# Kernel tuning notes

Hardware: AMD Instinct MI355X
Metric: run time of the kernel (lower is better)

The kernel has to match this reference:

```python
import jax, jax.numpy as jnp
import numpy as np

USER_NUM = 100000
ITEM_NUM = 50000
D = 64
E = 3200000
B = 16384


def setup_inputs() -> dict:
    key = jax.random.key(0)
    ks = jax.random.split(key, 12)
    user = jax.random.randint(ks[0], (B,), 0, USER_NUM)
    item_i = jax.random.randint(ks[1], (B,), 0, ITEM_NUM)
    item_j = jax.random.randint(ks[2], (B,), 0, ITEM_NUM)
    edge_u = jax.random.randint(ks[3], (E,), 0, USER_NUM)
    edge_i = jax.random.randint(ks[4], (E,), 0, ITEM_NUM)
    edge_val = jax.random.uniform(ks[5], (E,), dtype=jnp.float32)
    # nn.init.normal_(std=0.01)
    user_emb = 0.01 * jax.random.normal(ks[6], (USER_NUM, D), dtype=jnp.float32)
    item_emb = 0.01 * jax.random.normal(ks[7], (ITEM_NUM, D), dtype=jnp.float32)
    old_U_emb = 0.01 * jax.random.normal(ks[8], (USER_NUM, D), dtype=jnp.float32)
    old_I_emb = 0.01 * jax.random.normal(ks[9], (ITEM_NUM, D), dtype=jnp.float32)
    n_U = jax.random.uniform(ks[10], (USER_NUM,), dtype=jnp.float32)
    n_U = n_U / jnp.linalg.norm(n_U)  # pre_self normalizes by L2 norm
    n_I = jax.random.uniform(ks[11], (ITEM_NUM,), dtype=jnp.float32)
    n_I = n_I / jnp.linalg.norm(n_I)
    return {"user": user, "item_i": item_i, "item_j": item_j,
            "edge_u": edge_u, "edge_i": edge_i, "edge_val": edge_val,
            "user_emb": user_emb, "item_emb": item_emb,
            "old_U_emb": old_U_emb, "old_I_emb": old_I_emb,
            "n_U": n_U, "n_I": n_I}


def _spmm(seg_ids, gather_ids, vals, x, num_segments):
    # one hop of sparse adjacency @ dense embeddings: gather -> scale -> scatter-add
    msg = vals[:, None] * x[gather_ids]          # [E, D]
    return jax.ops.segment_sum(msg, seg_ids, num_segments=num_segments)


def reference(user, item_i, item_j, edge_u, edge_i, edge_val,
              user_emb, item_emb, old_U_emb, old_I_emb, n_U, n_I):
    # 3-hop LightGCN-style propagation over bipartite graph
    g1u = _spmm(edge_u, edge_i, edge_val, item_emb, USER_NUM)
    g1i = _spmm(edge_i, edge_u, edge_val, user_emb, ITEM_NUM)
    g2u = _spmm(edge_u, edge_i, edge_val, g1i, USER_NUM)
    g2i = _spmm(edge_i, edge_u, edge_val, g1u, ITEM_NUM)
    g3u = _spmm(edge_u, edge_i, edge_val, g2i, USER_NUM)
    g3i = _spmm(edge_i, edge_u, edge_val, g2u, ITEM_NUM)
    gcn_u = user_emb + 0.5 * g1u + (1.0 / 3.0) * g2u + 0.25 * g3u
    gcn_i = item_emb + 0.5 * g1i + (1.0 / 3.0) * g2i + 0.25 * g3i

    # BPR loss
    u = gcn_u[user]
    ii = gcn_i[item_i]
    ij = gcn_i[item_j]
    pred_i = jnp.sum(u * ii, axis=-1)
    pred_j = jnp.sum(u * ij, axis=-1)
    bpr = -jnp.mean(jax.nn.log_sigmoid(pred_i - pred_j))
    reg = 1e-4 * jnp.mean(jnp.sum(u ** 2 + ii ** 2 + ij ** 2, axis=-1))
    loss_bpr = bpr + reg

    # self-distillation loss (loss_self)
    Ud = jnp.linalg.norm(old_U_emb - gcn_u, axis=1)  # [USER_NUM]
    Id = jnp.linalg.norm(old_I_emb - gcn_i, axis=1)  # [ITEM_NUM]
    loss_self = jnp.dot(Ud, n_U) / USER_NUM + jnp.dot(Id, n_I) / ITEM_NUM

    return jnp.stack([loss_bpr, 100.0 * loss_self,
                      jnp.float32(1.0), jnp.float32(1.0)])
```

## Files before the change

kernel.cpp:

```cpp
#include <hip/hip_runtime.h>

#define USER_NUM 100000
#define ITEM_NUM 50000
#define DD 64
#define NEDGE 3200000
#define NB 16384
#define NSLOT 256

#define ATILE 4096
#define NTILE ((NEDGE + ATILE - 1) / ATILE)
#define USH 9
#define ISH 8
#define UBK ((USER_NUM + (1 << USH) - 1) >> USH)
#define IBK ((ITEM_NUM + (1 << ISH) - 1) >> ISH)
#define NBK (UBK + IBK)
#define CPAD 16
#define HIST_GRID 784

#define FP8_SCALE 64.0f

typedef float v2f __attribute__((ext_vector_type(2)));

__device__ __forceinline__ float waveReduceSum(float x) {
#pragma unroll
    for (int off = 32; off > 0; off >>= 1)
        x += __shfl_down(x, off, 64);
    return x;
}

__device__ __forceinline__ unsigned roundbf(unsigned y) {
    return (y + 0x7fffu + ((y >> 16) & 1u)) >> 16;
}

__device__ __forceinline__ void dec8(const uint2 b, float* f) {
    v2f f0 = __builtin_amdgcn_cvt_pk_f32_fp8(b.x, false);
    v2f f1 = __builtin_amdgcn_cvt_pk_f32_fp8(b.x, true);
    v2f f2 = __builtin_amdgcn_cvt_pk_f32_fp8(b.y, false);
    v2f f3 = __builtin_amdgcn_cvt_pk_f32_fp8(b.y, true);
    f[0] = f0.x; f[1] = f0.y; f[2] = f1.x; f[3] = f1.y;
    f[4] = f2.x; f[5] = f2.y; f[6] = f3.x; f[7] = f3.y;
}
__device__ __forceinline__ void fma8p(const uint2 b, const float v, v2f* a) {
    v2f f0 = __builtin_amdgcn_cvt_pk_f32_fp8(b.x, false);
    v2f f1 = __builtin_amdgcn_cvt_pk_f32_fp8(b.x, true);
    v2f f2 = __builtin_amdgcn_cvt_pk_f32_fp8(b.y, false);
    v2f f3 = __builtin_amdgcn_cvt_pk_f32_fp8(b.y, true);
    const v2f vv = {v, v};
    a[0] += vv * f0;
    a[1] += vv * f1;
    a[2] += vv * f2;
    a[3] += vv * f3;
}
__device__ __forceinline__ uint2 pack_fp8x8(const float* a) {
    int lo = 0, hi = 0;
    lo = __builtin_amdgcn_cvt_pk_fp8_f32(a[0], a[1], lo, false);
    lo = __builtin_amdgcn_cvt_pk_fp8_f32(a[2], a[3], lo, true);
    hi = __builtin_amdgcn_cvt_pk_fp8_f32(a[4], a[5], hi, false);
    hi = __builtin_amdgcn_cvt_pk_fp8_f32(a[6], a[7], hi, true);
    return make_uint2((unsigned)lo, (unsigned)hi);
}

__global__ void __launch_bounds__(256) cvt8_kernel(
    const float4* __restrict__ src, uint2* __restrict__ dst, int n8) {
    int t = blockIdx.x * blockDim.x + threadIdx.x;
    if (t < n8) {
        float4 a = src[2 * t], b = src[2 * t + 1];
        float f[8] = {a.x * FP8_SCALE, a.y * FP8_SCALE, a.z * FP8_SCALE, a.w * FP8_SCALE,
                      b.x * FP8_SCALE, b.y * FP8_SCALE, b.z * FP8_SCALE, b.w * FP8_SCALE};
        dst[t] = pack_fp8x8(f);
    }
}


__global__ void __launch_bounds__(256) coarse_hist(
    const int4* __restrict__ eu4, const int4* __restrict__ ei4,
    int* __restrict__ coarseCnt) {
    __shared__ int lc[NBK];
    const int t = threadIdx.x;
    for (int j = t; j < NBK; j += 256) lc[j] = 0;
    __syncthreads();
    for (int k = blockIdx.x * 256 + t; k < NEDGE / 4; k += HIST_GRID * 256) {
        int4 u = eu4[k];
        int4 i = ei4[k];
        atomicAdd(&lc[u.x >> USH], 1); atomicAdd(&lc[u.y >> USH], 1);
        atomicAdd(&lc[u.z >> USH], 1); atomicAdd(&lc[u.w >> USH], 1);
        atomicAdd(&lc[UBK + (i.x >> ISH)], 1); atomicAdd(&lc[UBK + (i.y >> ISH)], 1);
        atomicAdd(&lc[UBK + (i.z >> ISH)], 1); atomicAdd(&lc[UBK + (i.w >> ISH)], 1);
    }
    __syncthreads();
    for (int j = t; j < NBK; j += 256)
        if (lc[j]) atomicAdd(&coarseCnt[j * CPAD], lc[j]);
}

__global__ void __launch_bounds__(512) coarse_scan(
    const int* __restrict__ cnt, int* __restrict__ base, int* __restrict__ cur) {
    __shared__ int a[512];
    const int t = threadIdx.x;
    int v = (t < UBK) ? cnt[t * CPAD] : 0;
    a[t] = v;
    __syncthreads();
    for (int off = 1; off < 512; off <<= 1) {
        int x = (t >= off) ? a[t - off] : 0;
        __syncthreads();
        a[t] += x;
        __syncthreads();
    }
    if (t < UBK) { base[t] = a[t] - v; cur[t * CPAD] = a[t] - v; }
    __syncthreads();
    v = (t < IBK) ? cnt[(UBK + t) * CPAD] : 0;
    a[t] = v;
    __syncthreads();
    for (int off = 1; off < 512; off <<= 1) {
        int x = (t >= off) ? a[t - off] : 0;
        __syncthreads();
        a[t] += x;
        __syncthreads();
    }
    if (t < IBK) { base[UBK + t] = a[t] - v; cur[(UBK + t) * CPAD] = a[t] - v; }
}

__global__ void __launch_bounds__(256, 4) binA(
    const int* __restrict__ eu, const int* __restrict__ ei,
    const float* __restrict__ ev,
    int* __restrict__ ccur,
    int2* __restrict__ stU, int2* __restrict__ stI) {
    __shared__ int2 pay[ATILE];
    __shared__ unsigned char sbid[ATILE];
    __shared__ int hist[256];
    __shared__ int pscan[256];
    __shared__ int cursor[256];
    __shared__ int delta[256];

    const int t = threadIdx.x;
    const int dirI = blockIdx.y;
    const int tb = blockIdx.x * ATILE;
    const int n = min(ATILE, NEDGE - tb);
    const int* key = dirI ? ei : eu;
    const int SH = dirI ? ISH : USH;

    hist[t] = 0;
    __syncthreads();
    for (int k = t; k < n; k += 256)
        atomicAdd(&hist[key[tb + k] >> SH], 1);
    __syncthreads();
    pscan[t] = hist[t];
    __syncthreads();
    for (int off = 1; off < 256; off <<= 1) {
        int x = (t >= off) ? pscan[t - off] : 0;
        __syncthreads();
        pscan[t] += x;
        __syncthreads();
    }
    {
        const int c = hist[t];
        const int lst = pscan[t] - c;
        cursor[t] = lst;
        int gp = 0;
        if (c > 0) {
            int* gc = dirI ? (ccur + UBK * CPAD) : ccur;
            gp = atomicAdd(&gc[t * CPAD], c);
        }
        delta[t] = gp - lst;
    }
    __syncthreads();
    if (dirI == 0) {
        for (int k = t; k < n; k += 256) {
            const int e = tb + k;
            const int u = eu[e], i = ei[e];
            const int b = u >> USH;
            const int p = atomicAdd(&cursor[b], 1);
            pay[p] = make_int2(((u & ((1 << USH) - 1)) << 16) | i,
                               __float_as_int(ev[e]));
            sbid[p] = (unsigned char)b;
        }
    } else {
        for (int k = t; k < n; k += 256) {
            const int e = tb + k;
            const int u = eu[e], i = ei[e];
            const int b = i >> ISH;
            const int p = atomicAdd(&cursor[b], 1);
            pay[p] = make_int2(((i & ((1 << ISH) - 1)) << 17) | u,
                               __float_as_int(ev[e]));
            sbid[p] = (unsigned char)b;
        }
    }
    __syncthreads();
    int2* st = dirI ? stI : stU;
    for (int p = t; p < n; p += 256)
        st[delta[sbid[p]] + p] = pay[p];
}

__global__ void __launch_bounds__(256) binB(
    const int2* __restrict__ stU, const int2* __restrict__ stI,
    const int* __restrict__ base, const int* __restrict__ cnt,
    int* __restrict__ rpU, int* __restrict__ rpI,
    unsigned* __restrict__ ivU, unsigned* __restrict__ ivI) {
    __shared__ int h[512];
    const int t = threadIdx.x;
    const int b = blockIdx.x;
    if (b < UBK) {
        const int s = base[b], n = cnt[b * CPAD];
        const int dbase = b << USH;
        h[t] = 0; h[t + 256] = 0;
        __syncthreads();
        for (int p = s + t; p < s + n; p += 256)
            atomicAdd(&h[(unsigned)stU[p].x >> 16], 1);
        __syncthreads();
        int o0 = h[t], o1 = h[t + 256];
        for (int off = 1; off < 512; off <<= 1) {
            int x0 = (t >= off) ? h[t - off] : 0;
            int x1 = (t + 256 >= off) ? h[t + 256 - off] : 0;
            __syncthreads();
            h[t] += x0; h[t + 256] += x1;
            __syncthreads();
        }
        int e0 = s + h[t] - o0, e1 = s + h[t + 256] - o1;
        __syncthreads();
        h[t] = e0; h[t + 256] = e1;
        if (dbase + t < USER_NUM) rpU[dbase + t] = e0;
        if (dbase + 256 + t < USER_NUM) rpU[dbase + 256 + t] = e1;
        if (t == 0 && dbase + 512 >= USER_NUM) rpU[USER_NUM] = s + n;
        __syncthreads();
        for (int p = s + t; p < s + n; p += 256) {
            int2 en = stU[p];
            unsigned x = (unsigned)en.x;
            int pos = atomicAdd(&h[x >> 16], 1);
            unsigned bf = roundbf((unsigned)en.y);
            ivU[pos] = (bf << 16) | (x & 0xFFFFu);
        }
    } else {
        const int ib = b - UBK;
        const int s = base[b], n = cnt[b * CPAD];
        const int dbase = ib << ISH;
        h[t] = 0;
        __syncthreads();
        for (int p = s + t; p < s + n; p += 256)
            atomicAdd(&h[(unsigned)stI[p].x >> 17], 1);
        __syncthreads();
        int o0 = h[t];
        for (int off = 1; off < 256; off <<= 1) {
            int x0 = (t >= off) ? h[t - off] : 0;
            __syncthreads();
            h[t] += x0;
            __syncthreads();
        }
        int e0 = s + h[t] - o0;
        __syncthreads();
        h[t] = e0;
        if (dbase + t < ITEM_NUM) rpI[dbase + t] = e0;
        if (t == 0 && dbase + 256 >= ITEM_NUM) rpI[ITEM_NUM] = s + n;
        __syncthreads();
        for (int p = s + t; p < s + n; p += 256) {
            int2 en = stI[p];
            unsigned x = (unsigned)en.x;
            int pos = atomicAdd(&h[x >> 17], 1);
            unsigned v15 = roundbf((unsigned)en.y) & 0x7FFFu;
            ivI[pos] = (v15 << 17) | (x & 0x1FFFFu);
        }
    }
}

#define UW (USER_NUM / 8)
#define IW (ITEM_NUM / 8)

template<bool ISU>
__device__ __forceinline__ int xof(unsigned q) {
    return ISU ? (int)(q & 0xFFFFu) : (int)(q & 0x1FFFFu);
}
template<bool ISU>
__device__ __forceinline__ float vof(unsigned q) {
    return ISU ? __uint_as_float(q & 0xFFFF0000u)
               : __uint_as_float((q >> 17) << 16);
}

template<bool ISU, int N>
__device__ __forceinline__ void edge_block(
    const unsigned* __restrict__ iv, int t,
    const uint2* __restrict__ srcr, v2f* a0, v2f* a1) {
    unsigned q[N];
    uint2 b[N];
#pragma unroll
    for (int j = 0; j < N; j++) q[j] = iv[t + j];
#pragma unroll
    for (int j = 0; j < N; j++) b[j] = srcr[xof<ISU>(q[j]) * 8];
#pragma unroll
    for (int j = 0; j < N; j++) fma8p(b[j], vof<ISU>(q[j]), (j & 1) ? a1 : a0);
}

template<bool ISU>
__device__ __forceinline__ void row_accum_own(
    const int* __restrict__ rp, const unsigned* __restrict__ iv,
    const uint2* __restrict__ src, int row, int r, float* acc) {
    const int s = rp[row], e2 = rp[row + 1];
    const uint2* __restrict__ srcr = src + r;
    v2f a0[4] = {{0.f, 0.f}, {0.f, 0.f}, {0.f, 0.f}, {0.f, 0.f}};
    v2f a1[4] = {{0.f, 0.f}, {0.f, 0.f}, {0.f, 0.f}, {0.f, 0.f}};
    int t = s;
    for (; t + 15 < e2; t += 16) edge_block<ISU, 16>(iv, t, srcr, a0, a1);
    if (t + 7 < e2) { edge_block<ISU, 8>(iv, t, srcr, a0, a1); t += 8; }
    if (t + 3 < e2) { edge_block<ISU, 4>(iv, t, srcr, a0, a1); t += 4; }
    if (t + 1 < e2) { edge_block<ISU, 2>(iv, t, srcr, a0, a1); t += 2; }
    if (t < e2)     edge_block<ISU, 1>(iv, t, srcr, a0, a1);
#pragma unroll
    for (int k = 0; k < 4; k++) {
        const v2f sv = a0[k] + a1[k];
        acc[2 * k]     = sv.x;
        acc[2 * k + 1] = sv.y;
    }
}

__global__ void __launch_bounds__(256) gather_hop_f8(
    const int* __restrict__ rpU, const unsigned* __restrict__ ivU,
    const uint2* __restrict__ srcForU, uint2* __restrict__ outU,
    const int* __restrict__ rpI, const unsigned* __restrict__ ivI,
    const uint2* __restrict__ srcForI, uint2* __restrict__ outI) {
    const int lane = threadIdx.x & 63;
    const int sub = lane >> 3;
    const int r = lane & 7;
    const int wave = blockIdx.x * 4 + (threadIdx.x >> 6);
    float acc[8];
    if (wave < UW) {
        const int row = wave * 8 + sub;
        row_accum_own<true>(rpU, ivU, srcForU, row, r, acc);
        outU[row * 8 + r] = pack_fp8x8(acc);
    } else if (wave < UW + IW) {
        const int row = (wave - UW) * 8 + sub;
        row_accum_own<false>(rpI, ivI, srcForI, row, r, acc);
        outI[row * 8 + r] = pack_fp8x8(acc);
    }
}

__global__ void __launch_bounds__(256) gather_hop3(
    const int* __restrict__ rpU, const unsigned* __restrict__ ivU,
    const uint2* __restrict__ srcForU,
    const int* __restrict__ rpI, const unsigned* __restrict__ ivI,
    const uint2* __restrict__ srcForI,
    const float4* __restrict__ embU, const uint2* __restrict__ g1u,
    const uint2* __restrict__ g2u, float4* __restrict__ gcnU,
    const float4* __restrict__ embI, const uint2* __restrict__ g1i,
    const uint2* __restrict__ g2i, float4* __restrict__ gcnI,
    const float4* __restrict__ oldU4, const float4* __restrict__ oldI4,
    const float* __restrict__ nU, const float* __restrict__ nI,
    float* __restrict__ accs) {
    const int lane = threadIdx.x & 63;
    const int sub = lane >> 3;
    const int r = lane & 7;
    const int wave = blockIdx.x * 4 + (threadIdx.x >> 6);
    float acc[8];
    const float4* emb; const uint2* g1; const uint2* g2; float4* gcn; int row;
    const float4* old4; const float* nrm; bool isU;
    if (wave < UW) {
        row = wave * 8 + sub;
        row_accum_own<true>(rpU, ivU, srcForU, row, r, acc);
        emb = embU; g1 = g1u; g2 = g2u; gcn = gcnU;
        old4 = oldU4; nrm = nU; isU = true;
    } else if (wave < UW + IW) {
        row = (wave - UW) * 8 + sub;
        row_accum_own<false>(rpI, ivI, srcForI, row, r, acc);
        emb = embI; g1 = g1i; g2 = g2i; gcn = gcnI;
        old4 = oldI4; nrm = nI; isU = false;
    } else return;
    {
        const float C1 = 0.5f / FP8_SCALE;
        const float C2 = (1.0f / 3.0f) / FP8_SCALE;
        const float C3 = 0.25f / FP8_SCALE;
        float f1[8], f2[8];
        dec8(g1[row * 8 + r], f1);
        dec8(g2[row * 8 + r], f2);
        const float4 e0 = emb[row * 16 + 2 * r];
        const float4 e1 = emb[row * 16 + 2 * r + 1];
        float4 o0, o1;
        o0.x = e0.x + C1 * f1[0] + C2 * f2[0] + C3 * acc[0];
        o0.y = e0.y + C1 * f1[1] + C2 * f2[1] + C3 * acc[1];
        o0.z = e0.z + C1 * f1[2] + C2 * f2[2] + C3 * acc[2];
        o0.w = e0.w + C1 * f1[3] + C2 * f2[3] + C3 * acc[3];
        o1.x = e1.x + C1 * f1[4] + C2 * f2[4] + C3 * acc[4];
        o1.y = e1.y + C1 * f1[5] + C2 * f2[5] + C3 * acc[5];
        o1.z = e1.z + C1 * f1[6] + C2 * f2[6] + C3 * acc[6];
        o1.w = e1.w + C1 * f1[7] + C2 * f2[7] + C3 * acc[7];
        gcn[row * 16 + 2 * r] = o0;
        gcn[row * 16 + 2 * r + 1] = o1;
        const float4 d0 = old4[row * 16 + 2 * r];
        const float4 d1 = old4[row * 16 + 2 * r + 1];
        const float ex = d0.x - o0.x, ey = d0.y - o0.y;
        const float ez = d0.z - o0.z, ew = d0.w - o0.w;
        const float fx = d1.x - o1.x, fy = d1.y - o1.y;
        const float fz = d1.z - o1.z, fw = d1.w - o1.w;
        float ss = ex * ex + ey * ey + ez * ez + ew * ew
                 + fx * fx + fy * fy + fz * fz + fw * fw;
        ss += __shfl_xor(ss, 1, 64);
        ss += __shfl_xor(ss, 2, 64);
        ss += __shfl_xor(ss, 4, 64);
        float val = (r == 0) ? sqrtf(ss) * nrm[row] : 0.0f;
        val = waveReduceSum(val);
        if (lane == 0) {
            const int slot = wave & (NSLOT - 1);
            unsafeAtomicAdd(&accs[(isU ? 2 : 3) * NSLOT + slot], val);
        }
    }
}

__global__ void __launch_bounds__(256) bpr_loss(
    const int* __restrict__ user, const int* __restrict__ itemI,
    const int* __restrict__ itemJ,
    const float4* __restrict__ gcnU4, const float4* __restrict__ gcnI4,
    float* __restrict__ accs) {
    const int lane = threadIdx.x & 63;
    const int sub = lane >> 4;
    const int r = lane & 15;
    const int W = blockIdx.x * 4 + (threadIdx.x >> 6);
    const int NW = gridDim.x * 4;
    float accB = 0.0f, accR = 0.0f;
    for (int g = W; g < NB / 4; g += NW) {
        const int samp = g * 4 + sub;
        const int uu = user[samp], vi = itemI[samp], vj = itemJ[samp];
        const float4 u  = gcnU4[uu * 16 + r];
        const float4 xi = gcnI4[vi * 16 + r];
        const float4 xj = gcnI4[vj * 16 + r];
        float pi = u.x * xi.x + u.y * xi.y + u.z * xi.z + u.w * xi.w;
        float pj = u.x * xj.x + u.y * xj.y + u.z * xj.z + u.w * xj.w;
        float rg = u.x * u.x + u.y * u.y + u.z * u.z + u.w * u.w
                 + xi.x * xi.x + xi.y * xi.y + xi.z * xi.z + xi.w * xi.w
                 + xj.x * xj.x + xj.y * xj.y + xj.z * xj.z + xj.w * xj.w;
#pragma unroll
        for (int off = 1; off <= 8; off <<= 1) {
            pi += __shfl_xor(pi, off, 64);
            pj += __shfl_xor(pj, off, 64);
            rg += __shfl_xor(rg, off, 64);
        }
        if (r == 0) {
            const float x = pi - pj;
            accB += fmaxf(-x, 0.0f) + log1pf(expf(-fabsf(x)));
            accR += rg;
        }
    }
    accB = waveReduceSum(accB);
    accR = waveReduceSum(accR);
    if (lane == 0) {
        const int slot = W & (NSLOT - 1);
        unsafeAtomicAdd(&accs[0 * NSLOT + slot], accB);
        unsafeAtomicAdd(&accs[1 * NSLOT + slot], accR);
    }
}

__global__ void __launch_bounds__(64) finalize(const float* __restrict__ accs,
                                               float* __restrict__ out) {
    const int lane = threadIdx.x;
    float s[4];
#pragma unroll
    for (int k = 0; k < 4; k++) {
        float v = 0.0f;
        for (int j = lane; j < NSLOT; j += 64) v += accs[k * NSLOT + j];
        s[k] = waveReduceSum(v);
    }
    if (lane == 0) {
        const float loss_bpr = s[0] / NB + 1e-4f * (s[1] / NB);
        const float loss_self = s[2] / USER_NUM + s[3] / ITEM_NUM;
        out[0] = loss_bpr;
        out[1] = 100.0f * loss_self;
        out[2] = 1.0f;
        out[3] = 1.0f;
    }
}

extern "C" void kernel_launch(void* const* d_in, const int* in_sizes, int n_in,
                              void* d_out, int out_size, void* d_ws, size_t ws_size,
                              hipStream_t stream) {
    const int*   user     = (const int*)d_in[0];
    const int*   item_i   = (const int*)d_in[1];
    const int*   item_j   = (const int*)d_in[2];
    const int*   edge_u   = (const int*)d_in[3];
    const int*   edge_i   = (const int*)d_in[4];
    const float* edge_val = (const float*)d_in[5];
    const float* user_emb = (const float*)d_in[6];
    const float* item_emb = (const float*)d_in[7];
    const float* old_U    = (const float*)d_in[8];
    const float* old_I    = (const float*)d_in[9];
    const float* n_U      = (const float*)d_in[10];
    const float* n_I      = (const float*)d_in[11];
    float* out = (float*)d_out;

    char* base = (char*)d_ws;
    size_t off = 0;
    auto carve = [&](size_t bytes) {
        char* p = base + off;
        off += (bytes + 255) & ~(size_t)255;
        return p;
    };
    int*      coarseCnt = (int*)carve(NBK * CPAD * 4);
    float*    accs      = (float*)carve(4 * NSLOT * 4);
    size_t zero_bytes = off;
    int*      cbase = (int*)carve(NBK * 4);
    int*      ccur  = (int*)carve(NBK * CPAD * 4);
    int*      rpU   = (int*)carve((USER_NUM + 1) * 4);
    int*      rpI   = (int*)carve((ITEM_NUM + 1) * 4);
    unsigned* ivU   = (unsigned*)carve((size_t)NEDGE * 4);
    unsigned* ivI   = (unsigned*)carve((size_t)NEDGE * 4);
    uint2*    ebU8  = (uint2*)carve((size_t)USER_NUM * DD);
    uint2*    ebI8  = (uint2*)carve((size_t)ITEM_NUM * DD);
    uint2*    g1u8  = (uint2*)carve((size_t)USER_NUM * DD);
    uint2*    g1i8  = (uint2*)carve((size_t)ITEM_NUM * DD);
    uint2*    g2u8  = (uint2*)carve((size_t)USER_NUM * DD);
    uint2*    g2i8  = (uint2*)carve((size_t)ITEM_NUM * DD);
    int2*     stU   = (int2*)carve((size_t)NEDGE * 8);
    int2*     stI   = (int2*)carve((size_t)NEDGE * 8);
    float* gcnU = (float*)stU;
    float* gcnI = (float*)stI;

    hipMemsetAsync(d_ws, 0, zero_bytes, stream);

    const dim3 blk(256);

    cvt8_kernel<<<(USER_NUM * 8 + 255) / 256, blk, 0, stream>>>(
        (const float4*)user_emb, ebU8, USER_NUM * 8);
    cvt8_kernel<<<(ITEM_NUM * 8 + 255) / 256, blk, 0, stream>>>(
        (const float4*)item_emb, ebI8, ITEM_NUM * 8);

    coarse_hist<<<HIST_GRID, blk, 0, stream>>>((const int4*)edge_u,
                                               (const int4*)edge_i, coarseCnt);
    coarse_scan<<<1, 512, 0, stream>>>(coarseCnt, cbase, ccur);
    binA<<<dim3(NTILE, 2), blk, 0, stream>>>(edge_u, edge_i, edge_val,
                                             ccur, stU, stI);
    binB<<<NBK, blk, 0, stream>>>(stU, stI, cbase, coarseCnt, rpU, rpI, ivU, ivI);

    const int hop_waves = UW + IW;
    const int hop_grid = (hop_waves + 3) / 4;

    gather_hop_f8<<<hop_grid, blk, 0, stream>>>(rpU, ivU, ebI8, g1u8,
                                                rpI, ivI, ebU8, g1i8);
    gather_hop_f8<<<hop_grid, blk, 0, stream>>>(rpU, ivU, g1i8, g2u8,
                                                rpI, ivI, g1u8, g2i8);
    gather_hop3<<<hop_grid, blk, 0, stream>>>(
        rpU, ivU, g2i8, rpI, ivI, g2u8,
        (const float4*)user_emb, g1u8, g2u8, (float4*)gcnU,
        (const float4*)item_emb, g1i8, g2i8, (float4*)gcnI,
        (const float4*)old_U, (const float4*)old_I, n_U, n_I, accs);

    bpr_loss<<<128, blk, 0, stream>>>(user, item_i, item_j,
                                      (const float4*)gcnU, (const float4*)gcnI, accs);
    finalize<<<1, 64, 0, stream>>>(accs, out);
}
```

Measured before the change: 536.3 us.

## Sort rows by degree so each wave processes rows of similar length

```diff
diff --git a/kernel.cpp b/kernel.cpp
--- a/kernel.cpp
+++ b/kernel.cpp
@@ -16,6 +16,9 @@
 #define NBK (UBK + IBK)
 #define CPAD 16
 #define HIST_GRID 784
+#define PROWS 2048
+#define PBLK_U ((USER_NUM + PROWS - 1) / PROWS)
+#define PBLK_I ((ITEM_NUM + PROWS - 1) / PROWS)
 
 #define FP8_SCALE 64.0f
 
@@ -256,6 +259,96 @@
             int pos = atomicAdd(&h[x >> 17], 1);
             unsigned v15 = roundbf((unsigned)en.y) & 0x7FFFu;
             ivI[pos] = (v15 << 17) | (x & 0x1FFFFu);
+        }
+    }
+}
+
+
+__global__ void __launch_bounds__(256) perm_hist(
+    const int* __restrict__ rpU, const int* __restrict__ rpI,
+    int* __restrict__ bins) {
+    __shared__ int lb[512];
+    const int t = threadIdx.x;
+    for (int j = t; j < 512; j += 256) lb[j] = 0;
+    __syncthreads();
+    const int total = USER_NUM + ITEM_NUM;
+    for (int r = blockIdx.x * 256 + t; r < total; r += gridDim.x * 256) {
+        if (r < USER_NUM) {
+            const int d = rpU[r + 1] - rpU[r];
+            atomicAdd(&lb[255 - min(d, 255)], 1);
+        } else {
+            const int rr = r - USER_NUM;
+            const int d = rpI[rr + 1] - rpI[rr];
+            atomicAdd(&lb[256 + 255 - min(d, 255)], 1);
+        }
+    }
+    __syncthreads();
+    for (int j = t; j < 512; j += 256)
+        if (lb[j]) atomicAdd(&bins[j], lb[j]);
+}
+
+__global__ void __launch_bounds__(256) perm_scan(
+    const int* __restrict__ bins, int* __restrict__ gcur) {
+    __shared__ int a[256];
+    const int t = threadIdx.x;
+    int v = bins[t];
+    a[t] = v;
+    __syncthreads();
+    for (int off = 1; off < 256; off <<= 1) {
+        int x = (t >= off) ? a[t - off] : 0;
+        __syncthreads();
+        a[t] += x;
+        __syncthreads();
+    }
+    gcur[t * CPAD] = a[t] - v;
+    __syncthreads();
+    v = bins[256 + t];
+    a[t] = v;
+    __syncthreads();
+    for (int off = 1; off < 256; off <<= 1) {
+        int x = (t >= off) ? a[t - off] : 0;
+        __syncthreads();
+        a[t] += x;
+        __syncthreads();
+    }
+    gcur[(256 + t) * CPAD] = a[t] - v;
+}
+
+__global__ void __launch_bounds__(256) perm_scatter(
+    const int* __restrict__ rpU, const int* __restrict__ rpI,
+    int* __restrict__ gcur,
+    int* __restrict__ permU, int* __restrict__ permI) {
+    __shared__ int lh[256], lcur[256], ldelta[256];
+    const int t = threadIdx.x;
+    const int b = blockIdx.x;
+    const bool isU = b < PBLK_U;
+    const int r0 = (isU ? b : (b - PBLK_U)) * PROWS;
+    const int NR = isU ? USER_NUM : ITEM_NUM;
+    const int* __restrict__ rp = isU ? rpU : rpI;
+    int* __restrict__ perm = isU ? permU : permI;
+    int* __restrict__ cur = gcur + (isU ? 0 : 256 * CPAD);
+    lh[t] = 0; lcur[t] = 0;
+    __syncthreads();
+    for (int k = t; k < PROWS; k += 256) {
+        const int r = r0 + k;
+        if (r < NR) {
+            const int d = rp[r + 1] - rp[r];
+            atomicAdd(&lh[255 - min(d, 255)], 1);
+        }
+    }
+    __syncthreads();
+    {
+        const int c = lh[t];
+        ldelta[t] = c ? atomicAdd(&cur[t * CPAD], c) : 0;
+    }
+    __syncthreads();
+    for (int k = t; k < PROWS; k += 256) {
+        const int r = r0 + k;
+        if (r < NR) {
+            const int d = rp[r + 1] - rp[r];
+            const int bin = 255 - min(d, 255);
+            const int rank = atomicAdd(&lcur[bin], 1);
+            perm[ldelta[bin] + rank] = r;
         }
     }
 }
@@ -313,18 +406,19 @@
     const int* __restrict__ rpU, const unsigned* __restrict__ ivU,
     const uint2* __restrict__ srcForU, uint2* __restrict__ outU,
     const int* __restrict__ rpI, const unsigned* __restrict__ ivI,
-    const uint2* __restrict__ srcForI, uint2* __restrict__ outI) {
+    const uint2* __restrict__ srcForI, uint2* __restrict__ outI,
+    const int* __restrict__ permU, const int* __restrict__ permI) {
     const int lane = threadIdx.x & 63;
     const int sub = lane >> 3;
     const int r = lane & 7;
     const int wave = blockIdx.x * 4 + (threadIdx.x >> 6);
     float acc[8];
     if (wave < UW) {
-        const int row = wave * 8 + sub;
+        const int row = permU[wave * 8 + sub];
         row_accum_own<true>(rpU, ivU, srcForU, row, r, acc);
         outU[row * 8 + r] = pack_fp8x8(acc);
     } else if (wave < UW + IW) {
-        const int row = (wave - UW) * 8 + sub;
+        const int row = permI[(wave - UW) * 8 + sub];
         row_accum_own<false>(rpI, ivI, srcForI, row, r, acc);
         outI[row * 8 + r] = pack_fp8x8(acc);
     }
@@ -341,7 +435,8 @@
     const uint2* __restrict__ g2i, float4* __restrict__ gcnI,
     const float4* __restrict__ oldU4, const float4* __restrict__ oldI4,
     const float* __restrict__ nU, const float* __restrict__ nI,
-    float* __restrict__ accs) {
+    float* __restrict__ accs,
+    const int* __restrict__ permU, const int* __restrict__ permI) {
     const int lane = threadIdx.x & 63;
     const int sub = lane >> 3;
     const int r = lane & 7;
@@ -350,12 +445,12 @@
     const float4* emb; const uint2* g1; const uint2* g2; float4* gcn; int row;
     const float4* old4; const float* nrm; bool isU;
     if (wave < UW) {
-        row = wave * 8 + sub;
+        row = permU[wave * 8 + sub];
         row_accum_own<true>(rpU, ivU, srcForU, row, r, acc);
         emb = embU; g1 = g1u; g2 = g2u; gcn = gcnU;
         old4 = oldU4; nrm = nU; isU = true;
     } else if (wave < UW + IW) {
-        row = (wave - UW) * 8 + sub;
+        row = permI[(wave - UW) * 8 + sub];
         row_accum_own<false>(rpI, ivI, srcForI, row, r, acc);
         emb = embI; g1 = g1i; g2 = g2i; gcn = gcnI;
         old4 = oldI4; nrm = nI; isU = false;
@@ -489,11 +584,15 @@
     };
     int*      coarseCnt = (int*)carve(NBK * CPAD * 4);
     float*    accs      = (float*)carve(4 * NSLOT * 4);
+    int*      bins      = (int*)carve(512 * 4);
     size_t zero_bytes = off;
     int*      cbase = (int*)carve(NBK * 4);
     int*      ccur  = (int*)carve(NBK * CPAD * 4);
+    int*      gcur  = (int*)carve(512 * CPAD * 4);
     int*      rpU   = (int*)carve((USER_NUM + 1) * 4);
     int*      rpI   = (int*)carve((ITEM_NUM + 1) * 4);
+    int*      permU = (int*)carve(USER_NUM * 4);
+    int*      permI = (int*)carve(ITEM_NUM * 4);
     unsigned* ivU   = (unsigned*)carve((size_t)NEDGE * 4);
     unsigned* ivI   = (unsigned*)carve((size_t)NEDGE * 4);
     uint2*    ebU8  = (uint2*)carve((size_t)USER_NUM * DD);
@@ -523,18 +622,25 @@
                                              ccur, stU, stI);
     binB<<<NBK, blk, 0, stream>>>(stU, stI, cbase, coarseCnt, rpU, rpI, ivU, ivI);
 
+    perm_hist<<<128, blk, 0, stream>>>(rpU, rpI, bins);
+    perm_scan<<<1, blk, 0, stream>>>(bins, gcur);
+    perm_scatter<<<PBLK_U + PBLK_I, blk, 0, stream>>>(rpU, rpI, gcur, permU, permI);
+
     const int hop_waves = UW + IW;
     const int hop_grid = (hop_waves + 3) / 4;
 
     gather_hop_f8<<<hop_grid, blk, 0, stream>>>(rpU, ivU, ebI8, g1u8,
-                                                rpI, ivI, ebU8, g1i8);
+                                                rpI, ivI, ebU8, g1i8,
+                                                permU, permI);
     gather_hop_f8<<<hop_grid, blk, 0, stream>>>(rpU, ivU, g1i8, g2u8,
-                                                rpI, ivI, g1u8, g2i8);
+                                                rpI, ivI, g1u8, g2i8,
+                                                permU, permI);
     gather_hop3<<<hop_grid, blk, 0, stream>>>(
         rpU, ivU, g2i8, rpI, ivI, g2u8,
         (const float4*)user_emb, g1u8, g2u8, (float4*)gcnU,
         (const float4*)item_emb, g1i8, g2i8, (float4*)gcnI,
-        (const float4*)old_U, (const float4*)old_I, n_U, n_I, accs);
+        (const float4*)old_U, (const float4*)old_I, n_U, n_I, accs,
+        permU, permI);
 
     bpr_loss<<<128, blk, 0, stream>>>(user, item_i, item_j,
                                       (const float4*)gcnU, (const float4*)gcnI, accs);
```

Result: no change. 539.2 us (+0.6%).
